# Optimization experiments

Hardware: AMD Instinct MI355X
Metric: run time of the kernel (lower is better)

## Reference

```python
import jax, jax.numpy as jnp
import numpy as np

N = 512            # input_size == number of graph nodes (X = I_N)
B = 64             # batch_size
H1, H2, H3 = 128, 64, 32   # hidden3 + 16 must equal 32 + class_nums
OUT = 8            # output_size; OUT*OUT + OUT == 72 (controller out channels)
CLS = 16           # class_nums (one-hot task encoding is 16-dim)


def setup_inputs():
    key = jax.random.key(0)
    ks = jax.random.split(key, 20)

    def u(k, shape, fan_out):
        s = 1.0 / np.sqrt(fan_out)
        return jax.random.uniform(k, shape, jnp.float32, -s, s)

    inp = {
        "adj": jax.random.uniform(ks[0], (B, 2, N, N), jnp.float32),
        "task_id": jax.random.randint(ks[1], (B,), 0, CLS),
    }
    dims = [(N, H1), (H1, H2), (H2, H3), (H3, OUT)]
    i = 2
    for pref in ("p", "n"):
        for l, (fi, fo) in enumerate(dims, 1):
            inp[f"w{l}{pref}"] = u(ks[i], (fi, fo), fo); i += 1
            inp[f"b{l}{pref}"] = u(ks[i], (fo,), fo); i += 1
    # controller: Conv1d(H3+CLS, 72, kernel=1, bias=False) -> stored as [72, H3+CLS]
    inp["wc"] = jax.random.normal(ks[i], (OUT * OUT + OUT, H3 + CLS), jnp.float32) * np.sqrt(2.0 / (OUT * OUT + OUT))
    return inp


def _normalize(adj):
    # D^-1/2 (A + I) D^-1/2, fully vectorized over [B, 2] (original loops in Python)
    a = adj + jnp.eye(adj.shape[-1], dtype=adj.dtype)
    d = a.sum(-1) ** -0.5                       # [B,2,N]
    return d[..., :, None] * a * d[..., None, :]


def _leaky(x):
    return jnp.where(x >= 0, x, 0.2 * x)


def _gcn_branch(feat, ws, bs):
    # feat: [B,N,N] normalized adjacency; X = I_N so first support = W1
    x = jnp.eye(N, dtype=feat.dtype)
    for i, (w, b) in enumerate(zip(ws, bs)):
        x = jnp.matmul(feat, jnp.matmul(x, w)) + b   # [B,N,fo]
        if i < len(ws) - 1:
            x = _leaky(x)
        if i == len(ws) - 2:
            conv3 = x
    return conv3, x                                  # ([B,N,H3], [B,N,OUT])


def _dcl(conv3, task_enc, conv4, wc):
    # conv3: [B,N,H3]; conv4: [B,N,OUT]; task_enc: [B,CLS]
    x_feat = conv3.mean(axis=1)                       # AdaptiveAvgPool1d over nodes -> [B,H3]
    x_cond = jnp.concatenate([x_feat, task_enc], 1)   # [B,H3+CLS]
    params = x_cond @ wc.T                            # [B,72]
    w = params[:, :OUT * OUT].reshape(B, OUT, OUT)    # per-sample dynamic head weights
    b = params[:, OUT * OUT:]                         # [B,OUT]
    # head_inputs = conv4.view(1,-1,N) with groups=B grouped conv1d (kernel 1)
    head = conv4.reshape(B, OUT, N)
    logits = jnp.einsum('boi,bin->bon', w, head) + b[..., None]   # [B,OUT,N]
    return logits.reshape(B, N, OUT)                  # faithful to torch reshape(N_,H_,-1)


def _forward(adj, task_id, w1p, b1p, w2p, b2p, w3p, b3p, w4p, b4p,
             w1n, b1n, w2n, b2n, w3n, b3n, w4n, b4n, wc):
    adj_n = _normalize(adj)
    feat_p, feat_n = adj_n[:, 0], adj_n[:, 1]
    p3, p4 = _gcn_branch(feat_p, [w1p, w2p, w3p, w4p], [b1p, b2p, b3p, b4p])
    n3, n4 = _gcn_branch(feat_n, [w1n, w2n, w3n, w4n], [b1n, b2n, b3n, b4n])
    te = jax.nn.one_hot(task_id, CLS, dtype=adj.dtype)   # encoding_task
    lp = _dcl(p3, te, p4, wc)
    ln = _dcl(n3, te, n4, wc)
    cc = jnp.concatenate([lp, ln], -1).reshape(-1, 2, N, OUT)  # [B,2,N,OUT]
    # F.dropout treated as identity (eval-mode determinism for reference)
    xm = jnp.matmul(cc, jnp.swapaxes(cc, -1, -2))              # [B,2,N,N]
    return jax.nn.log_sigmoid(xm) * -1.0


def reference(adj, task_id, w1p, b1p, w2p, b2p, w3p, b3p, w4p, b4p,
              w1n, b1n, w2n, b2n, w3n, b3n, w4n, b4n, wc):
    return _forward(adj, task_id, w1p, b1p, w2p, b2p, w3p, b3p, w4p, b4p,
                    w1n, b1n, w2n, b2n, w3n, b3n, w4n, b4n, wc)
```

## Files before the change

### kernel.cpp

```cpp
#include <hip/hip_runtime.h>
#include <math.h>

#define NN 512
#define NBC 128

typedef __attribute__((ext_vector_type(8))) __bf16 v8bf;
typedef __attribute__((ext_vector_type(4))) float v4f;

__device__ __forceinline__ void bsplit(float v, unsigned short& h, unsigned short& l) {
    unsigned u  = __builtin_bit_cast(unsigned, v);
    unsigned hb = (u + 0x7fffu + ((u >> 16) & 1u)) & 0xffff0000u;
    float hf    = __builtin_bit_cast(float, hb);
    h = (unsigned short)(hb >> 16);
    float lof   = v - hf;
    unsigned ul = __builtin_bit_cast(unsigned, lof);
    l = (unsigned short)((ul + 0x7fffu + ((ul >> 16) & 1u)) >> 16);
}

__device__ __forceinline__ void gl_lds16(const unsigned short* g, unsigned short* l) {
    __builtin_amdgcn_global_load_lds(
        (const __attribute__((address_space(1))) void*)g,
        (__attribute__((address_space(3))) void*)l, 16, 0, 0);
}

__global__ __launch_bounds__(256) void k_rowsum(const float* __restrict__ adj,
                                                float* __restrict__ dinv) {
    int wave = blockIdx.x * 4 + (threadIdx.x >> 6);
    int lane = threadIdx.x & 63;
    const float4* row = (const float4*)(adj + (size_t)wave * NN);
    float4 v0 = row[lane], v1 = row[lane + 64];
    float s = v0.x + v0.y + v0.z + v0.w + v1.x + v1.y + v1.z + v1.w;
    #pragma unroll
    for (int off = 32; off; off >>= 1) s += __shfl_down(s, off, 64);
    if (lane == 0) dinv[wave] = rsqrtf(1.0f + s);
}

__global__ __launch_bounds__(256) void k_convert(const float* __restrict__ adj,
    const float* __restrict__ dinv, unsigned short* __restrict__ anh,
    unsigned short* __restrict__ anl)
{
    unsigned gid = blockIdx.x * 256 + threadIdx.x;
    unsigned e = gid * 4;
    unsigned bc = e >> 18, rem = e & 0x3ffffu;
    unsigned i = rem >> 9, j = rem & 511u;
    float4 a = *(const float4*)(adj + (size_t)e);
    float di = dinv[bc * NN + i];
    const float4 dj = *(const float4*)(dinv + bc * NN + j);
    float v0 = di * dj.x * (a.x + ((j + 0) == i ? 1.f : 0.f));
    float v1 = di * dj.y * (a.y + ((j + 1) == i ? 1.f : 0.f));
    float v2 = di * dj.z * (a.z + ((j + 2) == i ? 1.f : 0.f));
    float v3 = di * dj.w * (a.w + ((j + 3) == i ? 1.f : 0.f));
    ushort4 hh, ll;
    bsplit(v0, hh.x, ll.x); bsplit(v1, hh.y, ll.y);
    bsplit(v2, hh.z, ll.z); bsplit(v3, hh.w, ll.w);
    *(ushort4*)(anh + e) = hh;
    *(ushort4*)(anl + e) = ll;
}

struct WJob  { const float* w; unsigned short* dh; unsigned short* dl; int HI; int HO; int HOP; };
struct WJobs { WJob j[8]; };
__global__ __launch_bounds__(256) void k_wprep(WJobs jobs) {
    WJob jb = jobs.j[blockIdx.y];
    int idx = blockIdx.x * 256 + threadIdx.x;
    if (idx >= jb.HOP * jb.HI) return;
    int h = idx / jb.HI, p = idx % jb.HI;
    float v = (h < jb.HO) ? jb.w[p * jb.HO + h] : 0.f;
    unsigned short hh, ll; bsplit(v, hh, ll);
    jb.dh[idx] = hh; jb.dl[idx] = ll;
}

template<int BN, int OUTW, bool SHAREDZ, bool ACT, bool WBF>
__global__ __launch_bounds__(256, 3) void k_mfma(
    const unsigned short* __restrict__ anh_, const unsigned short* __restrict__ anl_,
    const unsigned short* __restrict__ zh_,  const unsigned short* __restrict__ zl_,
    const float* __restrict__ bp, const float* __restrict__ bn,
    float* __restrict__ xf, unsigned short* __restrict__ xh, unsigned short* __restrict__ xl)
{
    constexpr int WC    = (BN >= 32) ? 2 : 1;
    constexpr int WR    = 4 / WC;
    constexpr int RF    = 64 / (WR * 16);
    constexpr int C     = (BN / WC) / 16;
    constexpr int ASH   = 64 * 32;
    constexpr int ZSH   = BN * 32;
    constexpr int ZPOS  = BN * 4;
    constexpr int ZCALL = (ZPOS + 255) / 256;
    constexpr int BUFS  = 2 * ASH + 2 * ZSH;
    __shared__ __align__(16) unsigned short smem[2][BUFS];

    const int bc = blockIdx.y, rb = blockIdx.x;
    const int t = threadIdx.x, w = t >> 6, lane = t & 63;
    const int m0 = lane & 15, quad = lane >> 4;
    const int wr = w / WC, wc = w % WC;
    const int s = SHAREDZ ? (bc & 1) : bc;

    const int arow = t >> 2;
    const int aslot = (t & 3) ^ ((arow >> 1) & 3);
    const unsigned short* ga_h = anh_ + ((size_t)bc * NN + (size_t)rb * 64 + arow) * NN + aslot * 8;
    const unsigned short* ga_l = anl_ + ((size_t)bc * NN + (size_t)rb * 64 + arow) * NN + aslot * 8;
    const unsigned short* gz_h[ZCALL];
    const unsigned short* gz_l[ZCALL];
    #pragma unroll
    for (int q = 0; q < ZCALL; ++q) {
        int p = q * 256 + t;
        if (p >= ZPOS) p = 0;
        int zr = p >> 2, zs = (p & 3) ^ ((zr >> 1) & 3);
        gz_h[q] = zh_ + ((size_t)s * BN + zr) * NN + zs * 8;
        gz_l[q] = zl_ + ((size_t)s * BN + zr) * NN + zs * 8;
    }
    const int wbase = w * 512;

    int ra[RF]; int rz[C];
    #pragma unroll
    for (int r = 0; r < RF; ++r) {
        int rho = wr * (RF * 16) + r * 16 + m0;
        ra[r] = rho * 32 + ((quad ^ ((rho >> 1) & 3)) * 8);
    }
    #pragma unroll
    for (int c = 0; c < C; ++c) {
        int n = wc * (BN / WC) + c * 16 + m0;
        rz[c] = 2 * ASH + n * 32 + ((quad ^ ((n >> 1) & 3)) * 8);
    }

    v4f acc[RF][C];
    #pragma unroll
    for (int r = 0; r < RF; ++r)
        #pragma unroll
        for (int c = 0; c < C; ++c) acc[r][c] = (v4f){0.f, 0.f, 0.f, 0.f};

    auto STAGE = [&](int b, int kb) {
        const int ko = kb * 32;
        unsigned short* base = smem[b];
        gl_lds16(ga_h + ko, base + wbase);
        gl_lds16(ga_l + ko, base + ASH + wbase);
        #pragma unroll
        for (int q = 0; q < ZCALL; ++q) {
            if (q * 256 + w * 64 < ZPOS) {
                gl_lds16(gz_h[q] + ko, base + 2 * ASH + q * 2048 + wbase);
                gl_lds16(gz_l[q] + ko, base + 2 * ASH + ZSH + q * 2048 + wbase);
            }
        }
    };

    STAGE(0, 0);
    int buf = 0;
    for (int kb = 0; kb < 16; ++kb) {
        __syncthreads();
        if (kb < 15) STAGE(buf ^ 1, kb + 1);
        const unsigned short* bs = smem[buf];
        v8bf zfh[C], zfl[C];
        #pragma unroll
        for (int c = 0; c < C; ++c) {
            zfh[c] = *(const v8bf*)(bs + rz[c]);
            zfl[c] = *(const v8bf*)(bs + rz[c] + ZSH);
        }
        #pragma unroll
        for (int r = 0; r < RF; ++r) {
            v8bf ah = *(const v8bf*)(bs + ra[r]);
            v8bf al = *(const v8bf*)(bs + ra[r] + ASH);
            #pragma unroll
            for (int c = 0; c < C; ++c) {
                acc[r][c] = __builtin_amdgcn_mfma_f32_16x16x32_bf16(ah, zfh[c], acc[r][c], 0, 0, 0);
                acc[r][c] = __builtin_amdgcn_mfma_f32_16x16x32_bf16(ah, zfl[c], acc[r][c], 0, 0, 0);
                acc[r][c] = __builtin_amdgcn_mfma_f32_16x16x32_bf16(al, zfh[c], acc[r][c], 0, 0, 0);
            }
        }
        buf ^= 1;
    }

    const float* bias = (bc & 1) ? bn : bp;
    #pragma unroll
    for (int r = 0; r < RF; ++r)
        #pragma unroll
        for (int c = 0; c < C; ++c) {
            int col = wc * (BN / WC) + c * 16 + m0;
            if (OUTW < BN && col >= OUTW) continue;
            float bv = bias[col];
            #pragma unroll
            for (int reg = 0; reg < 4; ++reg) {
                int row = rb * 64 + wr * (RF * 16) + r * 16 + quad * 4 + reg;
                float v = acc[r][c][reg] + bv;
                if (ACT) v = v >= 0.f ? v : 0.2f * v;
                size_t oi = ((size_t)bc * NN + row) * OUTW + col;
                if (xf) xf[oi] = v;
                if (WBF) {
                    unsigned short hh, ll; bsplit(v, hh, ll);
                    xh[oi] = hh; xl[oi] = ll;
                }
            }
        }
}

template<int HI, int HOP>
__global__ __launch_bounds__(256) void k_zgemm(
    const unsigned short* __restrict__ wth, const unsigned short* __restrict__ wtl,
    const unsigned short* __restrict__ xh_, const unsigned short* __restrict__ xl_,
    unsigned short* __restrict__ zh_, unsigned short* __restrict__ zl_)
{
    constexpr int MT = HOP / 16, JW = 4 / MT, NT = 8 / JW;
    const int bc = blockIdx.y, jb = blockIdx.x;
    const int t = threadIdx.x, w = t >> 6, lane = t & 63;
    const int m0 = lane & 15, quad = lane >> 4;
    const int mt = w % MT, jseg = w / MT;
    const int n0 = jb * 128 + jseg * (128 / JW);
    const int s = bc & 1;
    const unsigned short* pw_h = wth + ((size_t)s * HOP + mt * 16 + m0) * HI + quad * 8;
    const unsigned short* pw_l = wtl + ((size_t)s * HOP + mt * 16 + m0) * HI + quad * 8;
    const unsigned short* px_h = xh_ + ((size_t)bc * NN + n0 + m0) * HI + quad * 8;
    const unsigned short* px_l = xl_ + ((size_t)bc * NN + n0 + m0) * HI + quad * 8;
    v4f acc[NT];
    #pragma unroll
    for (int c = 0; c < NT; ++c) acc[c] = (v4f){0.f, 0.f, 0.f, 0.f};
    #pragma unroll
    for (int ks = 0; ks < HI / 32; ++ks) {
        const int ko = ks * 32;
        v8bf awh = *(const v8bf*)(pw_h + ko);
        v8bf awl = *(const v8bf*)(pw_l + ko);
        #pragma unroll
        for (int c = 0; c < NT; ++c) {
            v8bf bxh = *(const v8bf*)(px_h + (size_t)(c * 16) * HI + ko);
            v8bf bxl = *(const v8bf*)(px_l + (size_t)(c * 16) * HI + ko);
            acc[c] = __builtin_amdgcn_mfma_f32_16x16x32_bf16(awh, bxh, acc[c], 0, 0, 0);
            acc[c] = __builtin_amdgcn_mfma_f32_16x16x32_bf16(awh, bxl, acc[c], 0, 0, 0);
            acc[c] = __builtin_amdgcn_mfma_f32_16x16x32_bf16(awl, bxh, acc[c], 0, 0, 0);
        }
    }
    #pragma unroll
    for (int c = 0; c < NT; ++c) {
        int j = n0 + c * 16 + m0;
        #pragma unroll
        for (int reg = 0; reg < 4; ++reg) {
            int h = mt * 16 + quad * 4 + reg;
            unsigned short hh, ll; bsplit(acc[c][reg], hh, ll);
            size_t oi = ((size_t)bc * HOP + h) * NN + j;
            zh_[oi] = hh; zl_[oi] = ll;
        }
    }
}

template<int H, int HP, bool SHARED, bool ACT>
__global__ __launch_bounds__(256) void k_biggemm(
    const float* __restrict__ adj, const float* __restrict__ zcg,
    const float* __restrict__ wp, const float* __restrict__ wn,
    const float* __restrict__ bp, const float* __restrict__ bn,
    const float* __restrict__ dinv, float* __restrict__ xout)
{
    constexpr int CPT = HP / 16;
    constexpr int KT = 64;
    __shared__ float a_s[64 * 68];
    __shared__ float z_s[KT * H];
    const int bc = blockIdx.y;
    const int rt = blockIdx.x;
    const int t  = threadIdx.x;
    const int tx = t & 15, ty = t >> 4;
    const float* A    = adj + (size_t)bc * NN * NN + (size_t)rt * 64 * NN;
    const float* dloc = dinv + bc * NN;
    const float* ZG   = SHARED ? ((bc & 1) ? wn : wp) : (zcg + (size_t)bc * NN * H);
    const float* bias = (bc & 1) ? bn : bp;
    float acc[4][CPT];
    #pragma unroll
    for (int r = 0; r < 4; ++r)
        #pragma unroll
        for (int u = 0; u < CPT; ++u) acc[r][u] = 0.f;
    for (int kb = 0; kb < NN; kb += KT) {
        __syncthreads();
        #pragma unroll
        for (int l = 0; l < 4; ++l) {
            int idx = t + l * 256;
            int r = idx >> 4, q = idx & 15;
            float4 v = *(const float4*)(A + (size_t)r * NN + kb + q * 4);
            *(float4*)(a_s + r * 68 + q * 4) = v;
        }
        constexpr int NZ4 = KT * H / 4;
        for (int idx = t; idx < NZ4; idx += 256) {
            int k = idx / (H / 4), hq = idx % (H / 4);
            float4 v = *(const float4*)(ZG + (size_t)(kb + k) * H + hq * 4);
            if (SHARED) {
                float dk = dloc[kb + k];
                v.x *= dk; v.y *= dk; v.z *= dk; v.w *= dk;
            }
            *(float4*)(z_s + k * H + hq * 4) = v;
        }
        __syncthreads();
        #pragma unroll 8
        for (int k = 0; k < KT; ++k) {
            float ar[4];
            #pragma unroll
            for (int r = 0; r < 4; ++r) ar[r] = a_s[(ty * 4 + r) * 68 + k];
            float zv[CPT];
            #pragma unroll
            for (int u = 0; u < CPT; ++u) {
                int h = tx * CPT + u;
                if (H < HP && h >= H) h = 0;
                zv[u] = z_s[k * H + h];
            }
            #pragma unroll
            for (int r = 0; r < 4; ++r)
                #pragma unroll
                for (int u = 0; u < CPT; ++u)
                    acc[r][u] += ar[r] * zv[u];
        }
    }
    #pragma unroll
    for (int r = 0; r < 4; ++r) {
        int i = rt * 64 + ty * 4 + r;
        float di = dloc[i];
        #pragma unroll
        for (int u = 0; u < CPT; ++u) {
            int h = tx * CPT + u;
            if (H < HP && h >= H) continue;
            float self = SHARED ? di * ZG[(size_t)i * H + h] : ZG[(size_t)i * H + h];
            float v = di * (acc[r][u] + self) + bias[h];
            if (ACT) v = v >= 0.f ? v : 0.2f * v;
            xout[((size_t)bc * NN + i) * H + h] = v;
        }
    }
}

template<int HI, int HO>
__global__ __launch_bounds__(256) void k_smallgemm(
    const float* __restrict__ xin, const float* __restrict__ wp,
    const float* __restrict__ wn, const float* __restrict__ dinv,
    float* __restrict__ zc)
{
    constexpr int CPT = (HO >= 16) ? HO / 16 : 1;
    constexpr int XS = HI + 4;
    __shared__ float x_s[32 * XS];
    __shared__ float w_s[HI * HO];
    const int bc = blockIdx.y, jt = blockIdx.x, t = threadIdx.x;
    const int tx = t & 15, ty = t >> 4;
    const float* W = (bc & 1) ? wn : wp;
    const float* X = xin + ((size_t)bc * NN + jt * 32) * HI;
    for (int idx = t; idx < HI * HO / 4; idx += 256)
        *(float4*)(w_s + idx * 4) = *(const float4*)(W + idx * 4);
    for (int idx = t; idx < 32 * HI / 4; idx += 256) {
        int r = idx / (HI / 4), q = idx % (HI / 4);
        *(float4*)(x_s + r * XS + q * 4) = *(const float4*)(X + (size_t)r * HI + q * 4);
    }
    __syncthreads();
    float acc[2][CPT];
    #pragma unroll
    for (int r = 0; r < 2; ++r)
        #pragma unroll
        for (int u = 0; u < CPT; ++u) acc[r][u] = 0.f;
    #pragma unroll 4
    for (int p = 0; p < HI; ++p) {
        float xr[2];
        #pragma unroll
        for (int r = 0; r < 2; ++r) xr[r] = x_s[(ty * 2 + r) * XS + p];
        float wv[CPT];
        #pragma unroll
        for (int u = 0; u < CPT; ++u) {
            int h = tx * CPT + u;
            if (HO < 16 && h >= HO) h = 0;
            wv[u] = w_s[p * HO + h];
        }
        #pragma unroll
        for (int r = 0; r < 2; ++r)
            #pragma unroll
            for (int u = 0; u < CPT; ++u) acc[r][u] += xr[r] * wv[u];
    }
    const float* dloc = dinv + bc * NN;
    #pragma unroll
    for (int r = 0; r < 2; ++r) {
        int j = jt * 32 + ty * 2 + r;
        float dj = dloc[j];
        #pragma unroll
        for (int u = 0; u < CPT; ++u) {
            int h = tx * CPT + u;
            if (HO < 16 && h >= HO) continue;
            zc[((size_t)bc * NN + j) * HO + h] = dj * acc[r][u];
        }
    }
}

__global__ __launch_bounds__(256) void k_dcl(
    const float* __restrict__ x3, const float* __restrict__ x4,
    const float* __restrict__ wc, const int* __restrict__ task,
    float* __restrict__ L)
{
    __shared__ float ps[8][32];
    __shared__ float xf[32];
    __shared__ float pr[72];
    const int bc = blockIdx.x, t = threadIdx.x;
    const float* X3 = x3 + (size_t)bc * NN * 32;
    {
        int col = t & 31, rg = t >> 5;
        float s = 0.f;
        for (int r = rg; r < NN; r += 8) s += X3[r * 32 + col];
        ps[rg][col] = s;
    }
    __syncthreads();
    if (t < 32) {
        float s = 0.f;
        #pragma unroll
        for (int g = 0; g < 8; ++g) s += ps[g][t];
        xf[t] = s * (1.0f / 512.0f);
    }
    __syncthreads();
    if (t < 72) {
        int tid = task[bc >> 1];
        const float* wr = wc + t * 48;
        float s = wr[32 + tid];
        #pragma unroll
        for (int j = 0; j < 32; ++j) s += wr[j] * xf[j];
        pr[t] = s;
    }
    __syncthreads();
    const float* X4 = x4 + (size_t)bc * 4096;
    float* Lb = L + (size_t)bc * 4096;
    #pragma unroll
    for (int rep = 0; rep < 2; ++rep) {
        int n = rep * 256 + t;
        float hi[8];
        #pragma unroll
        for (int i = 0; i < 8; ++i) hi[i] = X4[i * 512 + n];
        #pragma unroll
        for (int o = 0; o < 8; ++o) {
            float s = pr[64 + o];
            #pragma unroll
            for (int i = 0; i < 8; ++i) s += pr[o * 8 + i] * hi[i];
            Lb[o * 512 + n] = s;
        }
    }
}

#define SCP 520
__global__ __launch_bounds__(256) void k_final(const float* __restrict__ L,
                                               float* __restrict__ out)
{
    __shared__ float scT[8 * SCP];
    const int bcid = blockIdx.y;
    const int b = bcid >> 1, c = bcid & 1;
    const int nt = blockIdx.x, t = threadIdx.x;
    const float* Lp = L + (size_t)(b * 2) * 4096;
    const float* Ln = Lp + 4096;
    for (int rep = 0; rep < 16; ++rep) {
        int e = rep * 256 + t;
        int f = c * 4096 + e;
        int n = f >> 4, k = f & 15;
        float v = (k < 8) ? Lp[n * 8 + k] : Ln[n * 8 + k - 8];
        scT[(e & 7) * SCP + (e >> 3)] = v;
    }
    __syncthreads();
    const int tx = t & 63, ty = t >> 6;
    const int n0 = nt * 32 + ty * 8;
    float cn[8][8];
    #pragma unroll
    for (int o = 0; o < 8; ++o)
        #pragma unroll
        for (int i = 0; i < 8; ++i) cn[i][o] = scT[o * SCP + n0 + i];
    float* ob = out + (size_t)bcid * NN * NN;
    #pragma unroll 2
    for (int mg = 0; mg < 8; ++mg) {
        int m = tx + mg * 64;
        float cm[8];
        #pragma unroll
        for (int o = 0; o < 8; ++o) cm[o] = scT[o * SCP + m];
        #pragma unroll
        for (int i = 0; i < 8; ++i) {
            float s = 0.f;
            #pragma unroll
            for (int o = 0; o < 8; ++o) s += cn[i][o] * cm[o];
            float r = fmaxf(-s, 0.f) + __logf(1.0f + __expf(-fabsf(s)));
            ob[(size_t)(n0 + i) * NN + m] = r;
        }
    }
}

extern "C" void kernel_launch(void* const* d_in, const int* in_sizes, int n_in,
                              void* d_out, int out_size, void* d_ws, size_t ws_size,
                              hipStream_t stream)
{
    const float* adj = (const float*)d_in[0];
    const int*  task = (const int*)d_in[1];
    const float* w1p = (const float*)d_in[2];  const float* b1p = (const float*)d_in[3];
    const float* w2p = (const float*)d_in[4];  const float* b2p = (const float*)d_in[5];
    const float* w3p = (const float*)d_in[6];  const float* b3p = (const float*)d_in[7];
    const float* w4p = (const float*)d_in[8];  const float* b4p = (const float*)d_in[9];
    const float* w1n = (const float*)d_in[10]; const float* b1n = (const float*)d_in[11];
    const float* w2n = (const float*)d_in[12]; const float* b2n = (const float*)d_in[13];
    const float* w3n = (const float*)d_in[14]; const float* b3n = (const float*)d_in[15];
    const float* w4n = (const float*)d_in[16]; const float* b4n = (const float*)d_in[17];
    const float* wc  = (const float*)d_in[18];
    (void)in_sizes; (void)n_in; (void)out_size;

    const size_t NEED = 198004736ull;
    if (ws_size >= NEED) {
        char* base = (char*)d_ws;
        float*          dinv = (float*)(base + 0);
        unsigned short* anh  = (unsigned short*)(base + 262144);
        unsigned short* anl  = (unsigned short*)(base + 67371008);
        unsigned short* zt1h = (unsigned short*)(base + 134479872);
        unsigned short* zt1l = (unsigned short*)(base + 134742016);
        unsigned short* wt2h = (unsigned short*)(base + 135004160);
        unsigned short* wt2l = (unsigned short*)(base + 135036928);
        unsigned short* wt3h = (unsigned short*)(base + 135069696);
        unsigned short* wt3l = (unsigned short*)(base + 135077888);
        unsigned short* wt4h = (unsigned short*)(base + 135086080);
        unsigned short* wt4l = (unsigned short*)(base + 135088128);
        unsigned short* x1h  = (unsigned short*)(base + 135090176);
        unsigned short* x1l  = (unsigned short*)(base + 151867392);
        unsigned short* zt2h = (unsigned short*)(base + 168644608);
        unsigned short* zt2l = (unsigned short*)(base + 177033216);
        float*          x3f  = (float*)(base + 185421824);
        float*          x4f  = (float*)(base + 193810432);
        float*          L    = (float*)(base + 195907584);
        unsigned short* x2h = x1h,  *x2l = x1l;
        unsigned short* x3h = x1h,  *x3l = x1l;
        unsigned short* zt3h = zt2h, *zt3l = zt2l;
        unsigned short* zt4h = zt2h, *zt4l = zt2l;

        k_rowsum<<<dim3(NBC * NN / 4), 256, 0, stream>>>(adj, dinv);
        k_convert<<<dim3(32768), 256, 0, stream>>>(adj, dinv, anh, anl);
        WJobs jobs;
        jobs.j[0] = {w1p, zt1h,          zt1l,          512, 128, 128};
        jobs.j[1] = {w1n, zt1h + 65536,  zt1l + 65536,  512, 128, 128};
        jobs.j[2] = {w2p, wt2h,          wt2l,          128,  64,  64};
        jobs.j[3] = {w2n, wt2h + 8192,   wt2l + 8192,   128,  64,  64};
        jobs.j[4] = {w3p, wt3h,          wt3l,           64,  32,  32};
        jobs.j[5] = {w3n, wt3h + 2048,   wt3l + 2048,    64,  32,  32};
        jobs.j[6] = {w4p, wt4h,          wt4l,           32,   8,  16};
        jobs.j[7] = {w4n, wt4h + 512,    wt4l + 512,     32,   8,  16};
        k_wprep<<<dim3(256, 8), 256, 0, stream>>>(jobs);

        k_mfma<128, 128, true,  true,  true ><<<dim3(8, NBC), 256, 0, stream>>>(
            anh, anl, zt1h, zt1l, b1p, b1n, nullptr, x1h, x1l);
        k_zgemm<128, 64><<<dim3(4, NBC), 256, 0, stream>>>(wt2h, wt2l, x1h, x1l, zt2h, zt2l);
        k_mfma<64, 64, false, true,  true ><<<dim3(8, NBC), 256, 0, stream>>>(
            anh, anl, zt2h, zt2l, b2p, b2n, nullptr, x2h, x2l);
        k_zgemm<64, 32><<<dim3(4, NBC), 256, 0, stream>>>(wt3h, wt3l, x2h, x2l, zt3h, zt3l);
        k_mfma<32, 32, false, true,  true ><<<dim3(8, NBC), 256, 0, stream>>>(
            anh, anl, zt3h, zt3l, b3p, b3n, x3f, x3h, x3l);
        k_zgemm<32, 16><<<dim3(4, NBC), 256, 0, stream>>>(wt4h, wt4l, x3h, x3l, zt4h, zt4l);
        k_mfma<16, 8, false, false, false><<<dim3(8, NBC), 256, 0, stream>>>(
            anh, anl, zt4h, zt4l, b4p, b4n, x4f, nullptr, nullptr);
        k_dcl<<<dim3(NBC), 256, 0, stream>>>(x3f, x4f, wc, task, L);
        k_final<<<dim3(16, NBC), 256, 0, stream>>>(L, (float*)d_out);
    } else {
        float* ws   = (float*)d_ws;
        float* dinv = ws;
        float* XA   = ws + 65536;
        float* X3   = XA + 8388608;
        float* X4   = X3 + 2097152;
        float* L    = X4 + 524288;
        float* ZC   = L  + 524288;
        k_rowsum<<<dim3(NBC * NN / 4), 256, 0, stream>>>(adj, dinv);
        k_biggemm<128,128,true ,true ><<<dim3(8,128), 256, 0, stream>>>(adj, nullptr, w1p, w1n, b1p, b1n, dinv, XA);
        k_smallgemm<128,64><<<dim3(16,128), 256, 0, stream>>>(XA, w2p, w2n, dinv, ZC);
        k_biggemm<64,64,false,true ><<<dim3(8,128), 256, 0, stream>>>(adj, ZC, nullptr, nullptr, b2p, b2n, dinv, XA);
        k_smallgemm<64,32><<<dim3(16,128), 256, 0, stream>>>(XA, w3p, w3n, dinv, ZC);
        k_biggemm<32,32,false,true ><<<dim3(8,128), 256, 0, stream>>>(adj, ZC, nullptr, nullptr, b3p, b3n, dinv, X3);
        k_smallgemm<32,8><<<dim3(16,128), 256, 0, stream>>>(X3, w4p, w4n, dinv, ZC);
        k_biggemm<8,16,false,false><<<dim3(8,128), 256, 0, stream>>>(adj, ZC, nullptr, nullptr, b4p, b4n, dinv, X4);
        k_dcl<<<dim3(128), 256, 0, stream>>>(X3, X4, wc, task, L);
        k_final<<<dim3(16,128), 256, 0, stream>>>(L, (float*)d_out);
    }
}
```

Before: 534.3 us.

## Deepen k_mfma global-to-LDS prefetch pipeline with explicit vmcnt waits

Replaces the double-buffered k_mfma main loop with an NBUF-deep ring buffer (triple buffering for narrower Z tiles). Each stage waits with an explicit s_waitcnt vmcnt count and a raw s_barrier instead of __syncthreads, so more async global_load_lds traffic stays in flight. It also compacts the small-Z staging so only the needed lanes issue loads, and raises the occupancy hint to 4 for the two narrow layers. The extra buffers use more LDS, and manual vmcnt accounting is fragile if the compiler reorders or adds memory ops.

Result: faster. 518.7 us (-2.9%).

```diff
diff --git a/kernel.cpp b/kernel.cpp
--- a/kernel.cpp
+++ b/kernel.cpp
@@ -21,6 +21,11 @@
     __builtin_amdgcn_global_load_lds(
         (const __attribute__((address_space(1))) void*)g,
         (__attribute__((address_space(3))) void*)l, 16, 0, 0);
+}
+
+template<int N>
+__device__ __forceinline__ void vmwait() {
+    asm volatile("s_waitcnt vmcnt(%0)" :: "n"(N) : "memory");
 }
 
 __global__ __launch_bounds__(256) void k_rowsum(const float* __restrict__ adj,
@@ -69,8 +74,8 @@
     jb.dh[idx] = hh; jb.dl[idx] = ll;
 }
 
-template<int BN, int OUTW, bool SHAREDZ, bool ACT, bool WBF>
-__global__ __launch_bounds__(256, 3) void k_mfma(
+template<int BN, int OUTW, bool SHAREDZ, bool ACT, bool WBF, int MINW>
+__global__ __launch_bounds__(256, MINW) void k_mfma(
     const unsigned short* __restrict__ anh_, const unsigned short* __restrict__ anl_,
     const unsigned short* __restrict__ zh_,  const unsigned short* __restrict__ zl_,
     const float* __restrict__ bp, const float* __restrict__ bn,
@@ -83,9 +88,12 @@
     constexpr int ASH   = 64 * 32;
     constexpr int ZSH   = BN * 32;
     constexpr int ZPOS  = BN * 4;
-    constexpr int ZCALL = (ZPOS + 255) / 256;
+    constexpr int ZR    = (ZPOS >= 256) ? ZPOS / 256 : 1;
+    constexpr int U     = 2 + 2 * ZR;
+    constexpr int DEPTH = (BN == 128) ? 1 : 2;
+    constexpr int NBUF  = DEPTH + 1;
     constexpr int BUFS  = 2 * ASH + 2 * ZSH;
-    __shared__ __align__(16) unsigned short smem[2][BUFS];
+    __shared__ __align__(16) unsigned short smem[NBUF][BUFS];
 
     const int bc = blockIdx.y, rb = blockIdx.x;
     const int t = threadIdx.x, w = t >> 6, lane = t & 63;
@@ -97,15 +105,22 @@
     const int aslot = (t & 3) ^ ((arow >> 1) & 3);
     const unsigned short* ga_h = anh_ + ((size_t)bc * NN + (size_t)rb * 64 + arow) * NN + aslot * 8;
     const unsigned short* ga_l = anl_ + ((size_t)bc * NN + (size_t)rb * 64 + arow) * NN + aslot * 8;
-    const unsigned short* gz_h[ZCALL];
-    const unsigned short* gz_l[ZCALL];
-    #pragma unroll
-    for (int q = 0; q < ZCALL; ++q) {
-        int p = q * 256 + t;
-        if (p >= ZPOS) p = 0;
+    const unsigned short* gz_h[ZR];
+    const unsigned short* gz_l[ZR];
+    if constexpr (ZPOS >= 256) {
+        #pragma unroll
+        for (int q = 0; q < ZR; ++q) {
+            int p = q * 256 + t;
+            int zr = p >> 2, zs = (p & 3) ^ ((zr >> 1) & 3);
+            gz_h[q] = zh_ + ((size_t)s * BN + zr) * NN + zs * 8;
+            gz_l[q] = zl_ + ((size_t)s * BN + zr) * NN + zs * 8;
+        }
+    } else {
+        constexpr int CPW = ZPOS / 4;
+        int p = w * CPW + (lane & (CPW - 1));
         int zr = p >> 2, zs = (p & 3) ^ ((zr >> 1) & 3);
-        gz_h[q] = zh_ + ((size_t)s * BN + zr) * NN + zs * 8;
-        gz_l[q] = zl_ + ((size_t)s * BN + zr) * NN + zs * 8;
+        gz_h[0] = zh_ + ((size_t)s * BN + zr) * NN + zs * 8;
+        gz_l[0] = zl_ + ((size_t)s * BN + zr) * NN + zs * 8;
     }
     const int wbase = w * 512;
 
@@ -129,24 +144,37 @@
 
     auto STAGE = [&](int b, int kb) {
         const int ko = kb * 32;
-        unsigned short* base = smem[b];
+        unsigned short* base = (unsigned short*)smem[b];
         gl_lds16(ga_h + ko, base + wbase);
         gl_lds16(ga_l + ko, base + ASH + wbase);
-        #pragma unroll
-        for (int q = 0; q < ZCALL; ++q) {
-            if (q * 256 + w * 64 < ZPOS) {
+        if constexpr (ZPOS >= 256) {
+            #pragma unroll
+            for (int q = 0; q < ZR; ++q) {
                 gl_lds16(gz_h[q] + ko, base + 2 * ASH + q * 2048 + wbase);
                 gl_lds16(gz_l[q] + ko, base + 2 * ASH + ZSH + q * 2048 + wbase);
             }
+        } else {
+            constexpr int CPW = ZPOS / 4;
+            if (lane < CPW) {
+                gl_lds16(gz_h[0] + ko, base + 2 * ASH + w * CPW * 8);
+                gl_lds16(gz_l[0] + ko, base + 2 * ASH + ZSH + w * CPW * 8);
+            }
         }
     };
 
-    STAGE(0, 0);
-    int buf = 0;
+    #pragma unroll
+    for (int pp = 0; pp < DEPTH; ++pp) STAGE(pp, pp);
+
+    #pragma unroll
     for (int kb = 0; kb < 16; ++kb) {
-        __syncthreads();
-        if (kb < 15) STAGE(buf ^ 1, kb + 1);
-        const unsigned short* bs = smem[buf];
+        if (kb + DEPTH < 16) STAGE((kb + DEPTH) % NBUF, kb + DEPTH);
+        const int rem = 15 - kb;
+        if (rem >= DEPTH)      vmwait<U * DEPTH>();
+        else if (rem == 1)     vmwait<U>();
+        else                   vmwait<0>();
+        __builtin_amdgcn_s_barrier();
+        asm volatile("" ::: "memory");
+        const unsigned short* bs = (const unsigned short*)smem[kb % NBUF];
         v8bf zfh[C], zfl[C];
         #pragma unroll
         for (int c = 0; c < C; ++c) {
@@ -164,7 +192,8 @@
                 acc[r][c] = __builtin_amdgcn_mfma_f32_16x16x32_bf16(al, zfh[c], acc[r][c], 0, 0, 0);
             }
         }
-        buf ^= 1;
+        asm volatile("" ::: "memory");
+        __builtin_amdgcn_s_barrier();
     }
 
     const float* bias = (bc & 1) ? bn : bp;
@@ -523,16 +552,16 @@
         jobs.j[7] = {w4n, wt4h + 512,    wt4l + 512,     32,   8,  16};
         k_wprep<<<dim3(256, 8), 256, 0, stream>>>(jobs);
 
-        k_mfma<128, 128, true,  true,  true ><<<dim3(8, NBC), 256, 0, stream>>>(
+        k_mfma<128, 128, true,  true,  true,  3><<<dim3(8, NBC), 256, 0, stream>>>(
             anh, anl, zt1h, zt1l, b1p, b1n, nullptr, x1h, x1l);
         k_zgemm<128, 64><<<dim3(4, NBC), 256, 0, stream>>>(wt2h, wt2l, x1h, x1l, zt2h, zt2l);
-        k_mfma<64, 64, false, true,  true ><<<dim3(8, NBC), 256, 0, stream>>>(
+        k_mfma<64, 64, false, true,  true,  3><<<dim3(8, NBC), 256, 0, stream>>>(
             anh, anl, zt2h, zt2l, b2p, b2n, nullptr, x2h, x2l);
         k_zgemm<64, 32><<<dim3(4, NBC), 256, 0, stream>>>(wt3h, wt3l, x2h, x2l, zt3h, zt3l);
-        k_mfma<32, 32, false, true,  true ><<<dim3(8, NBC), 256, 0, stream>>>(
+        k_mfma<32, 32, false, true,  true,  4><<<dim3(8, NBC), 256, 0, stream>>>(
             anh, anl, zt3h, zt3l, b3p, b3n, x3f, x3h, x3l);
         k_zgemm<32, 16><<<dim3(4, NBC), 256, 0, stream>>>(wt4h, wt4l, x3h, x3l, zt4h, zt4l);
-        k_mfma<16, 8, false, false, false><<<dim3(8, NBC), 256, 0, stream>>>(
+        k_mfma<16, 8, false, false, false, 4><<<dim3(8, NBC), 256, 0, stream>>>(
             anh, anl, zt4h, zt4l, b4p, b4n, x4f, nullptr, nullptr);
         k_dcl<<<dim3(NBC), 256, 0, stream>>>(x3f, x4f, wc, task, L);
         k_final<<<dim3(16, NBC), 256, 0, stream>>>(L, (float*)d_out);
```

## Pre-layout Z operands in MFMA fragment order and deepen A-tile pipeline

Applied to the files above, without the earlier changes.

Weight prep and the small z-GEMM now store the Z operand directly in MFMA fragment order, so the big aggregation kernel loads each B fragment straight from global memory into registers instead of staging it through LDS. The LDS ring for the adjacency tiles grows to four buffers with three stages in flight, using explicit vmcnt waits and raw barriers in place of __syncthreads. Occupancy hints are raised for the smaller-width layers. This aims to cut LDS traffic and hide global latency, but relies on hand-counted vmcnt values and on every producer writing the new layout consistently.

Result: slower. 546.9 us (+2.4%).

```diff
diff --git a/kernel.cpp b/kernel.cpp
--- a/kernel.cpp
+++ b/kernel.cpp
@@ -21,6 +21,16 @@
     __builtin_amdgcn_global_load_lds(
         (const __attribute__((address_space(1))) void*)g,
         (__attribute__((address_space(3))) void*)l, 16, 0, 0);
+}
+
+template<int N>
+__device__ __forceinline__ void vmwait() {
+    asm volatile("s_waitcnt vmcnt(%0)" :: "n"(N) : "memory");
+}
+
+__device__ __forceinline__ size_t fragaddr(int n, int k, int kext) {
+    return ((size_t)(n >> 4) * (kext >> 5) + (k >> 5)) * 512
+         + (size_t)(((n & 15) + 16 * ((k >> 3) & 3)) * 8 + (k & 7));
 }
 
 __global__ __launch_bounds__(256) void k_rowsum(const float* __restrict__ adj,
@@ -57,7 +67,7 @@
     *(ushort4*)(anl + e) = ll;
 }
 
-struct WJob  { const float* w; unsigned short* dh; unsigned short* dl; int HI; int HO; int HOP; };
+struct WJob  { const float* w; unsigned short* dh; unsigned short* dl; int HI; int HO; int HOP; int frag; };
 struct WJobs { WJob j[8]; };
 __global__ __launch_bounds__(256) void k_wprep(WJobs jobs) {
     WJob jb = jobs.j[blockIdx.y];
@@ -66,60 +76,51 @@
     int h = idx / jb.HI, p = idx % jb.HI;
     float v = (h < jb.HO) ? jb.w[p * jb.HO + h] : 0.f;
     unsigned short hh, ll; bsplit(v, hh, ll);
-    jb.dh[idx] = hh; jb.dl[idx] = ll;
-}
-
-template<int BN, int OUTW, bool SHAREDZ, bool ACT, bool WBF>
-__global__ __launch_bounds__(256, 3) void k_mfma(
+    size_t oa = jb.frag ? fragaddr(h, p, jb.HI) : (size_t)idx;
+    jb.dh[oa] = hh; jb.dl[oa] = ll;
+}
+
+template<int BN, int OUTW, bool SHAREDZ, bool ACT, bool WBF, int MINW>
+__global__ __launch_bounds__(256, MINW) void k_mfma(
     const unsigned short* __restrict__ anh_, const unsigned short* __restrict__ anl_,
     const unsigned short* __restrict__ zh_,  const unsigned short* __restrict__ zl_,
     const float* __restrict__ bp, const float* __restrict__ bn,
     float* __restrict__ xf, unsigned short* __restrict__ xh, unsigned short* __restrict__ xl)
 {
-    constexpr int WC    = (BN >= 32) ? 2 : 1;
-    constexpr int WR    = 4 / WC;
-    constexpr int RF    = 64 / (WR * 16);
-    constexpr int C     = (BN / WC) / 16;
-    constexpr int ASH   = 64 * 32;
-    constexpr int ZSH   = BN * 32;
-    constexpr int ZPOS  = BN * 4;
-    constexpr int ZCALL = (ZPOS + 255) / 256;
-    constexpr int BUFS  = 2 * ASH + 2 * ZSH;
-    __shared__ __align__(16) unsigned short smem[2][BUFS];
+    constexpr int WC   = (BN >= 32) ? 2 : 1;
+    constexpr int WR   = 4 / WC;
+    constexpr int RF   = 64 / (WR * 16);
+    constexpr int C    = (BN / WC) / 16;
+    constexpr int ASH  = 64 * 32;
+    constexpr int NBUF = 4;
+    __shared__ __align__(16) unsigned short smem[NBUF][2 * ASH];
 
     const int bc = blockIdx.y, rb = blockIdx.x;
     const int t = threadIdx.x, w = t >> 6, lane = t & 63;
     const int m0 = lane & 15, quad = lane >> 4;
-    const int wr = w / WC, wc = w % WC;
+    const int wr = w / WC, wcc = w % WC;
     const int s = SHAREDZ ? (bc & 1) : bc;
 
     const int arow = t >> 2;
     const int aslot = (t & 3) ^ ((arow >> 1) & 3);
     const unsigned short* ga_h = anh_ + ((size_t)bc * NN + (size_t)rb * 64 + arow) * NN + aslot * 8;
     const unsigned short* ga_l = anl_ + ((size_t)bc * NN + (size_t)rb * 64 + arow) * NN + aslot * 8;
-    const unsigned short* gz_h[ZCALL];
-    const unsigned short* gz_l[ZCALL];
-    #pragma unroll
-    for (int q = 0; q < ZCALL; ++q) {
-        int p = q * 256 + t;
-        if (p >= ZPOS) p = 0;
-        int zr = p >> 2, zs = (p & 3) ^ ((zr >> 1) & 3);
-        gz_h[q] = zh_ + ((size_t)s * BN + zr) * NN + zs * 8;
-        gz_l[q] = zl_ + ((size_t)s * BN + zr) * NN + zs * 8;
-    }
     const int wbase = w * 512;
 
-    int ra[RF]; int rz[C];
+    const unsigned short* pzh[C]; const unsigned short* pzl[C];
+    #pragma unroll
+    for (int c = 0; c < C; ++c) {
+        int nt = (wcc * (BN / WC)) / 16 + c;
+        size_t zb = (size_t)s * BN * NN + (size_t)nt * (NN / 32) * 512 + (size_t)(lane * 8);
+        pzh[c] = zh_ + zb; pzl[c] = zl_ + zb;
+    }
+
+    int ra[RF];
     #pragma unroll
     for (int r = 0; r < RF; ++r) {
         int rho = wr * (RF * 16) + r * 16 + m0;
         ra[r] = rho * 32 + ((quad ^ ((rho >> 1) & 3)) * 8);
     }
-    #pragma unroll
-    for (int c = 0; c < C; ++c) {
-        int n = wc * (BN / WC) + c * 16 + m0;
-        rz[c] = 2 * ASH + n * 32 + ((quad ^ ((n >> 1) & 3)) * 8);
-    }
 
     v4f acc[RF][C];
     #pragma unroll
@@ -129,42 +130,44 @@
 
     auto STAGE = [&](int b, int kb) {
         const int ko = kb * 32;
-        unsigned short* base = smem[b];
-        gl_lds16(ga_h + ko, base + wbase);
-        gl_lds16(ga_l + ko, base + ASH + wbase);
-        #pragma unroll
-        for (int q = 0; q < ZCALL; ++q) {
-            if (q * 256 + w * 64 < ZPOS) {
-                gl_lds16(gz_h[q] + ko, base + 2 * ASH + q * 2048 + wbase);
-                gl_lds16(gz_l[q] + ko, base + 2 * ASH + ZSH + q * 2048 + wbase);
+        gl_lds16(ga_h + ko, &smem[b][0] + wbase);
+        gl_lds16(ga_l + ko, &smem[b][ASH] + wbase);
+    };
+
+    STAGE(0, 0); STAGE(1, 1); STAGE(2, 2);
+    asm volatile("" ::: "memory");
+    v8bf zrh[2][C], zrl[2][C];
+    #pragma unroll
+    for (int c = 0; c < C; ++c) { zrh[0][c] = *(const v8bf*)(pzh[c]); zrl[0][c] = *(const v8bf*)(pzl[c]); }
+
+    #pragma unroll
+    for (int kb = 0; kb < 16; ++kb) {
+        if (kb <= 13)      vmwait<4>();
+        else if (kb == 14) vmwait<2>();
+        else               vmwait<0>();
+        __builtin_amdgcn_s_barrier();
+        asm volatile("" ::: "memory");
+        if (kb + 3 < 16) STAGE((kb + 3) & 3, kb + 3);
+        const int cur = kb & 1, nxt = cur ^ 1;
+        if (kb + 1 < 16) {
+            #pragma unroll
+            for (int c = 0; c < C; ++c) {
+                zrh[nxt][c] = *(const v8bf*)(pzh[c] + (kb + 1) * 512);
+                zrl[nxt][c] = *(const v8bf*)(pzl[c] + (kb + 1) * 512);
             }
         }
-    };
-
-    STAGE(0, 0);
-    int buf = 0;
-    for (int kb = 0; kb < 16; ++kb) {
-        __syncthreads();
-        if (kb < 15) STAGE(buf ^ 1, kb + 1);
-        const unsigned short* bs = smem[buf];
-        v8bf zfh[C], zfl[C];
-        #pragma unroll
-        for (int c = 0; c < C; ++c) {
-            zfh[c] = *(const v8bf*)(bs + rz[c]);
-            zfl[c] = *(const v8bf*)(bs + rz[c] + ZSH);
-        }
+        const unsigned short* bs = &smem[kb & 3][0];
         #pragma unroll
         for (int r = 0; r < RF; ++r) {
             v8bf ah = *(const v8bf*)(bs + ra[r]);
-            v8bf al = *(const v8bf*)(bs + ra[r] + ASH);
+            v8bf al = *(const v8bf*)(bs + ASH + ra[r]);
             #pragma unroll
             for (int c = 0; c < C; ++c) {
-                acc[r][c] = __builtin_amdgcn_mfma_f32_16x16x32_bf16(ah, zfh[c], acc[r][c], 0, 0, 0);
-                acc[r][c] = __builtin_amdgcn_mfma_f32_16x16x32_bf16(ah, zfl[c], acc[r][c], 0, 0, 0);
-                acc[r][c] = __builtin_amdgcn_mfma_f32_16x16x32_bf16(al, zfh[c], acc[r][c], 0, 0, 0);
+                acc[r][c] = __builtin_amdgcn_mfma_f32_16x16x32_bf16(ah, zrh[cur][c], acc[r][c], 0, 0, 0);
+                acc[r][c] = __builtin_amdgcn_mfma_f32_16x16x32_bf16(ah, zrl[cur][c], acc[r][c], 0, 0, 0);
+                acc[r][c] = __builtin_amdgcn_mfma_f32_16x16x32_bf16(al, zrh[cur][c], acc[r][c], 0, 0, 0);
             }
         }
-        buf ^= 1;
     }
 
     const float* bias = (bc & 1) ? bn : bp;
@@ -172,7 +175,7 @@
     for (int r = 0; r < RF; ++r)
         #pragma unroll
         for (int c = 0; c < C; ++c) {
-            int col = wc * (BN / WC) + c * 16 + m0;
+            int col = wcc * (BN / WC) + c * 16 + m0;
             if (OUTW < BN && col >= OUTW) continue;
             float bv = bias[col];
             #pragma unroll
@@ -231,7 +234,7 @@
         for (int reg = 0; reg < 4; ++reg) {
             int h = mt * 16 + quad * 4 + reg;
             unsigned short hh, ll; bsplit(acc[c][reg], hh, ll);
-            size_t oi = ((size_t)bc * HOP + h) * NN + j;
+            size_t oi = (size_t)bc * HOP * NN + fragaddr(h, j, NN);
             zh_[oi] = hh; zl_[oi] = ll;
         }
     }
@@ -513,26 +516,26 @@
         k_rowsum<<<dim3(NBC * NN / 4), 256, 0, stream>>>(adj, dinv);
         k_convert<<<dim3(32768), 256, 0, stream>>>(adj, dinv, anh, anl);
         WJobs jobs;
-        jobs.j[0] = {w1p, zt1h,          zt1l,          512, 128, 128};
-        jobs.j[1] = {w1n, zt1h + 65536,  zt1l + 65536,  512, 128, 128};
-        jobs.j[2] = {w2p, wt2h,          wt2l,          128,  64,  64};
-        jobs.j[3] = {w2n, wt2h + 8192,   wt2l + 8192,   128,  64,  64};
-        jobs.j[4] = {w3p, wt3h,          wt3l,           64,  32,  32};
-        jobs.j[5] = {w3n, wt3h + 2048,   wt3l + 2048,    64,  32,  32};
-        jobs.j[6] = {w4p, wt4h,          wt4l,           32,   8,  16};
-        jobs.j[7] = {w4n, wt4h + 512,    wt4l + 512,     32,   8,  16};
+        jobs.j[0] = {w1p, zt1h,          zt1l,          512, 128, 128, 1};
+        jobs.j[1] = {w1n, zt1h + 65536,  zt1l + 65536,  512, 128, 128, 1};
+        jobs.j[2] = {w2p, wt2h,          wt2l,          128,  64,  64, 0};
+        jobs.j[3] = {w2n, wt2h + 8192,   wt2l + 8192,   128,  64,  64, 0};
+        jobs.j[4] = {w3p, wt3h,          wt3l,           64,  32,  32, 0};
+        jobs.j[5] = {w3n, wt3h + 2048,   wt3l + 2048,    64,  32,  32, 0};
+        jobs.j[6] = {w4p, wt4h,          wt4l,           32,   8,  16, 0};
+        jobs.j[7] = {w4n, wt4h + 512,    wt4l + 512,     32,   8,  16, 0};
         k_wprep<<<dim3(256, 8), 256, 0, stream>>>(jobs);
 
-        k_mfma<128, 128, true,  true,  true ><<<dim3(8, NBC), 256, 0, stream>>>(
+        k_mfma<128, 128, true,  true,  true,  3><<<dim3(8, NBC), 256, 0, stream>>>(
             anh, anl, zt1h, zt1l, b1p, b1n, nullptr, x1h, x1l);
         k_zgemm<128, 64><<<dim3(4, NBC), 256, 0, stream>>>(wt2h, wt2l, x1h, x1l, zt2h, zt2l);
-        k_mfma<64, 64, false, true,  true ><<<dim3(8, NBC), 256, 0, stream>>>(
+        k_mfma<64, 64, false, true,  true,  4><<<dim3(8, NBC), 256, 0, stream>>>(
             anh, anl, zt2h, zt2l, b2p, b2n, nullptr, x2h, x2l);
         k_zgemm<64, 32><<<dim3(4, NBC), 256, 0, stream>>>(wt3h, wt3l, x2h, x2l, zt3h, zt3l);
-        k_mfma<32, 32, false, true,  true ><<<dim3(8, NBC), 256, 0, stream>>>(
+        k_mfma<32, 32, false, true,  true,  4><<<dim3(8, NBC), 256, 0, stream>>>(
             anh, anl, zt3h, zt3l, b3p, b3n, x3f, x3h, x3l);
         k_zgemm<32, 16><<<dim3(4, NBC), 256, 0, stream>>>(wt4h, wt4l, x3h, x3l, zt4h, zt4l);
-        k_mfma<16, 8, false, false, false><<<dim3(8, NBC), 256, 0, stream>>>(
+        k_mfma<16, 8, false, false, false, 4><<<dim3(8, NBC), 256, 0, stream>>>(
             anh, anl, zt4h, zt4l, b4p, b4n, x4f, nullptr, nullptr);
         k_dcl<<<dim3(NBC), 256, 0, stream>>>(x3f, x4f, wc, task, L);
         k_final<<<dim3(16, NBC), 256, 0, stream>>>(L, (float*)d_out);
```
